# Kernel tuning notes

Hardware: AMD Instinct MI355X
Metric: run time of the kernel (lower is better)

Reference implementation:

```python
import jax, jax.numpy as jnp
import numpy as np

D_MODEL = 1024
N_HEADS = 16
HEAD_DIM = D_MODEL // N_HEADS
BATCH = 1
SEQLEN = 4096


def setup_inputs() -> dict:
    key = jax.random.key(0)
    k1, k2, k3 = jax.random.split(key, 3)
    x = jax.random.normal(k1, (BATCH, SEQLEN, D_MODEL), dtype=jnp.float32)
    # match typical Dense init scale so softmax isn't saturated
    Wqkv = jax.random.normal(k2, (D_MODEL, 3 * D_MODEL), dtype=jnp.float32) / np.sqrt(D_MODEL)
    Wout = jax.random.normal(k3, (D_MODEL, D_MODEL), dtype=jnp.float32) / np.sqrt(D_MODEL)
    return {"x": x, "Wqkv": Wqkv, "Wout": Wout}


def reference(x, Wqkv, Wout):
    b, l, d = x.shape
    qkv = x @ Wqkv  # [b, l, 3d]
    q, k, v = jnp.split(qkv, 3, axis=-1)
    # [b, l, d] -> [b, h, l, hd]
    def to_heads(t):
        return t.reshape(b, l, N_HEADS, HEAD_DIM).transpose(0, 2, 1, 3)
    q, k, v = to_heads(q), to_heads(k), to_heads(v)
    scale = 1.0 / np.sqrt(HEAD_DIM)
    attn = jnp.einsum('bhld,bhsd->bhls', q, k) * scale  # [b,h,l,l]
    causal_mask = jnp.tril(jnp.ones((l, l), dtype=bool))
    attn = jnp.where(causal_mask, attn, -jnp.inf)
    attn = jax.nn.softmax(attn, axis=-1)
    out = jnp.einsum('bhls,bhsd->bhld', attn, v)  # [b,h,l,hd]
    out = out.transpose(0, 2, 1, 3).reshape(b, l, d)
    return out @ Wout
```

## Files before the change

### kernel.cpp

```cpp
#include <hip/hip_runtime.h>

#define SEQ 4096
#define DM 1024
#define NH 16
#define HD 64

typedef __attribute__((ext_vector_type(8))) short short8;
typedef __attribute__((ext_vector_type(4))) short short4v;
typedef __attribute__((ext_vector_type(2))) short short2v;
typedef __attribute__((ext_vector_type(4))) float float4v;
typedef __attribute__((ext_vector_type(4))) int int4v;

__device__ __forceinline__ short f2bf(float f) {
    union { float f; unsigned u; } v; v.f = f;
    unsigned u = v.u;
    return (short)((u + 0x7fffu + ((u >> 16) & 1u)) >> 16);
}
__device__ __forceinline__ int cvtpk(float lo, float hi) {
    int r;
    asm("v_cvt_pk_bf16_f32 %0, %1, %2" : "=v"(r) : "v"(lo), "v"(hi));
    return r;
}

__device__ __forceinline__ void gload_lds16(const void* g, void* l) {
    __builtin_amdgcn_global_load_lds(
        (const __attribute__((address_space(1))) void*)g,
        (__attribute__((address_space(3))) void*)l, 16, 0, 0);
}

__global__ void cast_x(const float* __restrict__ in, short* __restrict__ out, int n4) {
    int i = blockIdx.x * blockDim.x + threadIdx.x;
    if (i < n4) {
        float4v x = ((const float4v*)in)[i];
        short4v o;
        o[0] = f2bf(x[0]); o[1] = f2bf(x[1]); o[2] = f2bf(x[2]); o[3] = f2bf(x[3]);
        ((short4v*)out)[i] = o;
    }
}

__global__ void transpose_cast(const float* __restrict__ in, short* __restrict__ out,
                               int H, int W, int scaled_rows, float scale) {
    __shared__ float tile[32][33];
    int bx = blockIdx.x * 32, by = blockIdx.y * 32;
    int tx = threadIdx.x, ty = threadIdx.y;
#pragma unroll
    for (int i = 0; i < 32; i += 8)
        tile[ty + i][tx] = in[(by + ty + i) * W + bx + tx];
    __syncthreads();
#pragma unroll
    for (int i = 0; i < 32; i += 8) {
        int orow = bx + ty + i;
        float sc = (orow < scaled_rows) ? scale : 1.0f;
        out[orow * H + by + tx] = f2bf(tile[tx][ty + i] * sc);
    }
}

__global__ void transpose_v(const short* __restrict__ qkv, short* __restrict__ vt) {
    __shared__ short tile[64][66];
    int h = blockIdx.z;
    int l0 = blockIdx.x * 64;
    int tx = threadIdx.x, ty = threadIdx.y;
#pragma unroll
    for (int i = 0; i < 8; i++) {
        int r = ty + i * 8;
        short2v v = *(const short2v*)&qkv[(l0 + r) * (3 * DM) + 2 * DM + h * HD + 2 * tx];
        tile[r][2 * tx] = v[0];
        tile[r][2 * tx + 1] = v[1];
    }
    __syncthreads();
#pragma unroll
    for (int i = 0; i < 8; i++) {
        int d = ty + i * 8;
        short2v v;
        v[0] = tile[2 * tx][d];
        v[1] = tile[2 * tx + 1][d];
        int s = l0 + 2 * tx;
        int soff = (s & ~31) | ((s & 12) << 1) | ((s & 16) >> 2) | (s & 3);
        *(short2v*)&vt[(h * HD + d) * SEQ + soff] = v;
    }
}

template <typename OutT>
__global__ __launch_bounds__(256) void gemm_bt(const short* __restrict__ A,
                                               const short* __restrict__ BT,
                                               OutT* __restrict__ C,
                                               int M, int N, int K) {
    __shared__ short As[128 * 32];
    __shared__ short Bs[128 * 32];
    int tid  = threadIdx.x;
    int m0   = blockIdx.y * 128;
    int n0   = blockIdx.x * 128;
    int w    = tid >> 6, lane = tid & 63;
    int wm   = w >> 1,  wn   = w & 1;
    int quad = lane >> 4, l15 = lane & 15;
    int srow = lane >> 2;
    int scol = (lane & 3) * 8;

    float4v acc[4][4];
#pragma unroll
    for (int mi = 0; mi < 4; mi++)
#pragma unroll
        for (int ni = 0; ni < 4; ni++)
            acc[mi][ni] = {0.f, 0.f, 0.f, 0.f};

    for (int k0 = 0; k0 < K; k0 += 32) {
        __syncthreads();
#pragma unroll
        for (int t = 0; t < 2; t++) {
            int chunk = w * 2 + t;
            int r = chunk * 16 + srow;
            gload_lds16(&A[(m0 + r) * K + k0 + scol], &As[chunk * 16 * 32]);
            gload_lds16(&BT[(n0 + r) * K + k0 + scol], &Bs[chunk * 16 * 32]);
        }
        __syncthreads();
        short8 a[4], b[4];
#pragma unroll
        for (int mi = 0; mi < 4; mi++)
            a[mi] = *(const short8*)&As[(wm * 64 + mi * 16 + l15) * 32 + quad * 8];
#pragma unroll
        for (int ni = 0; ni < 4; ni++)
            b[ni] = *(const short8*)&Bs[(wn * 64 + ni * 16 + l15) * 32 + quad * 8];
#pragma unroll
        for (int mi = 0; mi < 4; mi++)
#pragma unroll
            for (int ni = 0; ni < 4; ni++)
                acc[mi][ni] = __builtin_amdgcn_mfma_f32_16x16x32_bf16(a[mi], b[ni], acc[mi][ni], 0, 0, 0);
    }

#pragma unroll
    for (int mi = 0; mi < 4; mi++)
#pragma unroll
        for (int ni = 0; ni < 4; ni++)
#pragma unroll
            for (int r = 0; r < 4; r++) {
                int row = m0 + wm * 64 + mi * 16 + quad * 4 + r;
                int col = n0 + wn * 64 + ni * 16 + l15;
                float v = acc[mi][ni][r];
                if constexpr (sizeof(OutT) == 2) C[row * N + col] = (OutT)f2bf(v);
                else                             C[row * N + col] = (OutT)v;
            }
}

__global__ __launch_bounds__(256) void gemm_bt64(const short* __restrict__ A,
                                                 const short* __restrict__ BT,
                                                 float* __restrict__ C,
                                                 int M, int N, int K) {
    __shared__ short As[64 * 32];
    __shared__ short Bs[128 * 32];
    int tid  = threadIdx.x;
    int m0   = blockIdx.y * 64;
    int n0   = blockIdx.x * 128;
    int w    = tid >> 6, lane = tid & 63;
    int wm   = w >> 1,  wn   = w & 1;
    int quad = lane >> 4, l15 = lane & 15;
    int srow = lane >> 2;
    int scol = (lane & 3) * 8;

    float4v acc[2][4];
#pragma unroll
    for (int mi = 0; mi < 2; mi++)
#pragma unroll
        for (int ni = 0; ni < 4; ni++)
            acc[mi][ni] = {0.f, 0.f, 0.f, 0.f};

    for (int k0 = 0; k0 < K; k0 += 32) {
        __syncthreads();
        {
            int r = w * 16 + srow;
            gload_lds16(&A[(m0 + r) * K + k0 + scol], &As[w * 16 * 32]);
        }
#pragma unroll
        for (int t = 0; t < 2; t++) {
            int chunk = w * 2 + t;
            int r = chunk * 16 + srow;
            gload_lds16(&BT[(n0 + r) * K + k0 + scol], &Bs[chunk * 16 * 32]);
        }
        __syncthreads();
        short8 a[2], b[4];
#pragma unroll
        for (int mi = 0; mi < 2; mi++)
            a[mi] = *(const short8*)&As[(wm * 32 + mi * 16 + l15) * 32 + quad * 8];
#pragma unroll
        for (int ni = 0; ni < 4; ni++)
            b[ni] = *(const short8*)&Bs[(wn * 64 + ni * 16 + l15) * 32 + quad * 8];
#pragma unroll
        for (int mi = 0; mi < 2; mi++)
#pragma unroll
            for (int ni = 0; ni < 4; ni++)
                acc[mi][ni] = __builtin_amdgcn_mfma_f32_16x16x32_bf16(a[mi], b[ni], acc[mi][ni], 0, 0, 0);
    }

#pragma unroll
    for (int mi = 0; mi < 2; mi++)
#pragma unroll
        for (int ni = 0; ni < 4; ni++)
#pragma unroll
            for (int r = 0; r < 4; r++) {
                int row = m0 + wm * 32 + mi * 16 + quad * 4 + r;
                int col = n0 + wn * 64 + ni * 16 + l15;
                C[row * N + col] = acc[mi][ni][r];
            }
}

__global__ __launch_bounds__(256, 2) void attn_kernel(const short* __restrict__ qkv,
                                                      const short* __restrict__ vtp,
                                                      float* __restrict__ Of0,
                                                      float* __restrict__ Of1,
                                                      float* __restrict__ Of2,
                                                      float* __restrict__ Lf0,
                                                      float* __restrict__ Lf1,
                                                      float* __restrict__ Lf2) {
    __shared__ short Ks[3][64 * 64];
    __shared__ short Vs[3][64 * 64];
    int gid = blockIdx.x;
    int rr = gid & 7, qq = gid >> 3;
    int hb = qq / 48;
    int rem = qq - hb * 48;
    int h = rr + 8 * hb;
    int b = rem & 15;
    int j = rem >> 4;
    float* __restrict__ Of = (j == 0) ? Of0 : (j == 1) ? Of1 : Of2;
    float* __restrict__ Lf = (j == 0) ? Lf0 : (j == 1) ? Lf1 : Lf2;
    int B0 = 2 * b + 2;

    int tid = threadIdx.x;
    int w = tid >> 6, lane = tid & 63;
    int quad = lane >> 4, l15 = lane & 15;
    int rowb = w * 16;
    int lrow = lane >> 3;
    int cg   = (lane & 7) ^ lrow;
    int xr   = (l15 & 7) * 8;

    const short* Kg = qkv + DM + h * HD;
    const short* Vg = vtp + (h * HD) * SEQ;

    short8 onesv;
#pragma unroll
    for (int i = 0; i < 8; i++) onesv[i] = (short)0x3F80;

#pragma unroll 1
    for (int sg = 0; sg < 2; sg++) {
        int t, st0, stN;
        if (sg == 0) {
            t = b;
            st0 = 22 * j;
            stN = (22 * j + 22 < B0) ? 22 * j + 22 : B0;
        } else {
            t = 31 - b;
            int a0 = 22 * j - B0;
            st0 = (a0 > 0) ? a0 : 0;
            stN = 22 * j + 22 - B0;
        }
        if (st0 >= stN) continue;

        int q0 = t * 128;
        int qw = q0 + w * 32;

        short8 aq[2][2];
#pragma unroll
        for (int mi = 0; mi < 2; mi++)
#pragma unroll
            for (int kk = 0; kk < 2; kk++)
                aq[mi][kk] = *(const short8*)&qkv[(qw + mi * 16 + l15) * (3 * DM) + h * HD + kk * 32 + quad * 8];

        float4v lacc[2];
        float4v o[2][4];
#pragma unroll
        for (int mi = 0; mi < 2; mi++) {
            lacc[mi] = {0.f, 0.f, 0.f, 0.f};
#pragma unroll
            for (int dt = 0; dt < 4; dt++)
                o[mi][dt] = {0.f, 0.f, 0.f, 0.f};
        }

        auto stage = [&](int slot, int tt_) {
            int s0_ = tt_ * 64;
#pragma unroll
            for (int i = 0; i < 2; i++) {
                int r = rowb + i * 8;
                gload_lds16(&Kg[(s0_ + r + lrow) * (3 * DM) + cg * 8], &Ks[slot][r * 64]);
                gload_lds16(&Vg[(r + lrow) * SEQ + s0_ + cg * 8],      &Vs[slot][r * 64]);
            }
        };

        stage(0, st0);
        bool two = (st0 + 1 < stN);
        if (two) {
            stage(1, st0 + 1);
            asm volatile("s_waitcnt vmcnt(4)" ::: "memory");
        } else {
            asm volatile("s_waitcnt vmcnt(0)" ::: "memory");
        }
        __builtin_amdgcn_s_barrier();
        __builtin_amdgcn_sched_barrier(0);

        short8 pa_p[2][2];
        short8 vc_p[8];
        int si = 0;
        for (int tt = st0; tt < stN; tt++) {
            int s0 = tt * 64;
            int s2 = si + 2; if (s2 >= 3) s2 -= 3;
            bool haveStage = (tt + 2 < stN);
            if (haveStage) stage(s2, tt + 2);

            const short* Kb = &Ks[si][0];
            const short* Vb = &Vs[si][0];

            short8 kc[8];
#pragma unroll
            for (int ni = 0; ni < 4; ni++)
#pragma unroll
                for (int kk = 0; kk < 2; kk++)
                    kc[ni * 2 + kk] = *(const short8*)&Kb[(ni * 16 + l15) * 64 + (((kk * 4 + quad) * 8) ^ xr)];

            if (tt > st0) {
                __builtin_amdgcn_s_setprio(1);
#pragma unroll
                for (int mi = 0; mi < 2; mi++)
#pragma unroll
                    for (int pr = 0; pr < 2; pr++)
                        lacc[mi] = __builtin_amdgcn_mfma_f32_16x16x32_bf16(pa_p[mi][pr], onesv, lacc[mi], 0, 0, 0);
#pragma unroll
                for (int mi = 0; mi < 2; mi++)
#pragma unroll
                    for (int dt = 0; dt < 4; dt++)
#pragma unroll
                        for (int pr = 0; pr < 2; pr++)
                            o[mi][dt] = __builtin_amdgcn_mfma_f32_16x16x32_bf16(pa_p[mi][pr], vc_p[dt * 2 + pr], o[mi][dt], 0, 0, 0);
                __builtin_amdgcn_s_setprio(0);
            }

#pragma unroll
            for (int dt = 0; dt < 4; dt++)
#pragma unroll
                for (int pr = 0; pr < 2; pr++)
                    vc_p[dt * 2 + pr] = *(const short8*)&Vb[(dt * 16 + l15) * 64 + (((pr * 4 + quad) * 8) ^ xr)];

            float4v s[2][4];
            __builtin_amdgcn_s_setprio(1);
#pragma unroll
            for (int mi = 0; mi < 2; mi++)
#pragma unroll
                for (int ni = 0; ni < 4; ni++) {
                    float4v a = {0.f, 0.f, 0.f, 0.f};
#pragma unroll
                    for (int kk = 0; kk < 2; kk++)
                        a = __builtin_amdgcn_mfma_f32_16x16x32_bf16(kc[ni * 2 + kk], aq[mi][kk], a, 0, 0, 0);
                    s[mi][ni] = a;
                }
            __builtin_amdgcn_s_setprio(0);

            bool diag = (s0 + 63 > qw);
            if (diag) {
#pragma unroll
                for (int mi = 0; mi < 2; mi++) {
                    int qrow = qw + mi * 16 + l15;
#pragma unroll
                    for (int ni = 0; ni < 4; ni++)
#pragma unroll
                        for (int r = 0; r < 4; r++) {
                            float p = __builtin_amdgcn_exp2f(s[mi][ni][r]);
                            int scol = s0 + ni * 16 + quad * 4 + r;
                            s[mi][ni][r] = (scol <= qrow) ? p : 0.f;
                        }
                }
            } else {
#pragma unroll
                for (int mi = 0; mi < 2; mi++)
#pragma unroll
                    for (int ni = 0; ni < 4; ni++)
#pragma unroll
                        for (int r = 0; r < 4; r++)
                            s[mi][ni][r] = __builtin_amdgcn_exp2f(s[mi][ni][r]);
            }
#pragma unroll
            for (int mi = 0; mi < 2; mi++)
#pragma unroll
                for (int pr = 0; pr < 2; pr++) {
                    int4v wpk;
                    wpk[0] = cvtpk(s[mi][2 * pr][0], s[mi][2 * pr][1]);
                    wpk[1] = cvtpk(s[mi][2 * pr][2], s[mi][2 * pr][3]);
                    wpk[2] = cvtpk(s[mi][2 * pr + 1][0], s[mi][2 * pr + 1][1]);
                    wpk[3] = cvtpk(s[mi][2 * pr + 1][2], s[mi][2 * pr + 1][3]);
                    pa_p[mi][pr] = *(short8*)&wpk;
                }

            asm volatile("s_waitcnt lgkmcnt(0)" ::: "memory");
            if (haveStage) asm volatile("s_waitcnt vmcnt(4)" ::: "memory");
            else           asm volatile("s_waitcnt vmcnt(0)" ::: "memory");
            __builtin_amdgcn_s_barrier();
            __builtin_amdgcn_sched_barrier(0);
            si = si + 1; if (si >= 3) si = 0;
        }

        __builtin_amdgcn_s_setprio(1);
#pragma unroll
        for (int mi = 0; mi < 2; mi++)
#pragma unroll
            for (int pr = 0; pr < 2; pr++)
                lacc[mi] = __builtin_amdgcn_mfma_f32_16x16x32_bf16(pa_p[mi][pr], onesv, lacc[mi], 0, 0, 0);
#pragma unroll
        for (int mi = 0; mi < 2; mi++)
#pragma unroll
            for (int dt = 0; dt < 4; dt++)
#pragma unroll
                for (int pr = 0; pr < 2; pr++)
                    o[mi][dt] = __builtin_amdgcn_mfma_f32_16x16x32_bf16(pa_p[mi][pr], vc_p[dt * 2 + pr], o[mi][dt], 0, 0, 0);
        __builtin_amdgcn_s_setprio(0);

#pragma unroll
        for (int mi = 0; mi < 2; mi++)
#pragma unroll
            for (int r = 0; r < 4; r++) {
                int row = qw + mi * 16 + quad * 4 + r;
#pragma unroll
                for (int dt = 0; dt < 4; dt++)
                    Of[row * DM + h * HD + dt * 16 + l15] = o[mi][dt][r];
            }
        if (l15 == 0) {
#pragma unroll
            for (int mi = 0; mi < 2; mi++)
#pragma unroll
                for (int r = 0; r < 4; r++)
                    Lf[h * SEQ + qw + mi * 16 + quad * 4 + r] = lacc[mi][r];
        }
    }
}

__global__ void attn_finalize(const float* __restrict__ Of0, const float* __restrict__ Of1,
                              const float* __restrict__ Of2,
                              const float* __restrict__ Lf0, const float* __restrict__ Lf1,
                              const float* __restrict__ Lf2,
                              short* __restrict__ ao) {
    int i = blockIdx.x * blockDim.x + threadIdx.x;
    int q  = i >> 8;
    int c4 = i & 255;
    int h  = c4 >> 4;
    int t  = q >> 7;
    bool lowq = (t < 16);
    int b = lowq ? t : 31 - t;
    bool use0 = lowq || (b <= 9);
    bool use1 = (!lowq) || (b >= 11);
    bool use2 = !lowq;

    float l = 0.f;
    float4v acc = {0.f, 0.f, 0.f, 0.f};
    if (use0) {
        l += Lf0[h * SEQ + q];
        float4v a = ((const float4v*)Of0)[i];
        acc[0] += a[0]; acc[1] += a[1]; acc[2] += a[2]; acc[3] += a[3];
    }
    if (use1) {
        l += Lf1[h * SEQ + q];
        float4v a = ((const float4v*)Of1)[i];
        acc[0] += a[0]; acc[1] += a[1]; acc[2] += a[2]; acc[3] += a[3];
    }
    if (use2) {
        l += Lf2[h * SEQ + q];
        float4v a = ((const float4v*)Of2)[i];
        acc[0] += a[0]; acc[1] += a[1]; acc[2] += a[2]; acc[3] += a[3];
    }
    float inv = 1.0f / l;
    short4v o;
    o[0] = f2bf(acc[0] * inv);
    o[1] = f2bf(acc[1] * inv);
    o[2] = f2bf(acc[2] * inv);
    o[3] = f2bf(acc[3] * inv);
    ((short4v*)ao)[i] = o;
}

extern "C" void kernel_launch(void* const* d_in, const int* in_sizes, int n_in,
                              void* d_out, int out_size, void* d_ws, size_t ws_size,
                              hipStream_t stream) {
    const float* x    = (const float*)d_in[0];
    const float* Wqkv = (const float*)d_in[1];
    const float* Wout = (const float*)d_in[2];
    float* out = (float*)d_out;

    char* ws = (char*)d_ws;
    short* xb    = (short*)(ws);
    short* wqkvT = (short*)(ws + 8388608);
    float* Of0   = (float*)(ws);
    float* Of1   = (float*)(d_out);
    short* qkv   = (short*)(ws + 16777216);
    short* vt    = (short*)(ws + 41943040);
    short* ao    = (short*)(ws + 50331648);
    float* Of2   = (float*)(ws + 58720256);
    float* Lf0   = (float*)(ws + 75497472);
    float* Lf1   = (float*)(ws + 75759616);
    float* Lf2   = (float*)(ws + 76021760);
    short* woutT = (short*)(ws + 76283904);

    const float SC = 0.18033688011112042f;

    cast_x<<<4096, 256, 0, stream>>>(x, xb, (SEQ * DM) / 4);
    transpose_cast<<<dim3(3 * DM / 32, DM / 32), dim3(32, 8), 0, stream>>>(Wqkv, wqkvT, DM, 3 * DM, DM, SC);
    transpose_cast<<<dim3(DM / 32, DM / 32), dim3(32, 8), 0, stream>>>(Wout, woutT, DM, DM, 0, 1.0f);

    gemm_bt<short><<<dim3(3 * DM / 128, SEQ / 128), 256, 0, stream>>>(xb, wqkvT, qkv, SEQ, 3 * DM, DM);

    transpose_v<<<dim3(SEQ / 64, 1, NH), dim3(32, 8), 0, stream>>>(qkv, vt);

    attn_kernel<<<768, 256, 0, stream>>>(qkv, vt, Of0, Of1, Of2, Lf0, Lf1, Lf2);
    attn_finalize<<<(SEQ * DM / 4) / 256, 256, 0, stream>>>(Of0, Of1, Of2, Lf0, Lf1, Lf2, ao);

    gemm_bt64<<<dim3(DM / 128, SEQ / 64), 256, 0, stream>>>(ao, woutT, out, SEQ, DM, DM);
}
```

Measured before the change: 204.0 us.

## Split attention tile into halves interleaving QK, PV MFMAs and softmax; compute row sums on VALU

Splits each 64-key tile's QK^T, exp and PV work into two 32-column halves, with sched_barriers so the MFMAs of one half overlap the exp/pack work and V fragment loads of the other. The softmax denominator was computed with extra MFMAs against a ones vector. It now comes from per-lane VALU accumulation plus a cross-quad shuffle reduction at the end. This frees matrix-core cycles and shortens dependency chains, in exchange for more VALU adds and rigid scheduling that may limit compiler freedom.

```diff
diff --git a/kernel.cpp b/kernel.cpp
--- a/kernel.cpp
+++ b/kernel.cpp
@@ -234,10 +234,6 @@
     const short* Kg = qkv + DM + h * HD;
     const short* Vg = vtp + (h * HD) * SEQ;
 
-    short8 onesv;
-#pragma unroll
-    for (int i = 0; i < 8; i++) onesv[i] = (short)0x3F80;
-
 #pragma unroll 1
     for (int sg = 0; sg < 2; sg++) {
         int t, st0, stN;
@@ -263,15 +259,13 @@
             for (int kk = 0; kk < 2; kk++)
                 aq[mi][kk] = *(const short8*)&qkv[(qw + mi * 16 + l15) * (3 * DM) + h * HD + kk * 32 + quad * 8];
 
-        float4v lacc[2];
+        float lp[2] = {0.f, 0.f};
         float4v o[2][4];
 #pragma unroll
-        for (int mi = 0; mi < 2; mi++) {
-            lacc[mi] = {0.f, 0.f, 0.f, 0.f};
+        for (int mi = 0; mi < 2; mi++)
 #pragma unroll
             for (int dt = 0; dt < 4; dt++)
                 o[mi][dt] = {0.f, 0.f, 0.f, 0.f};
-        }
 
         auto stage = [&](int slot, int tt_) {
             int s0_ = tt_ * 64;
@@ -301,10 +295,12 @@
             int s0 = tt * 64;
             int s2 = si + 2; if (s2 >= 3) s2 -= 3;
             bool haveStage = (tt + 2 < stN);
+            bool havePrev  = (tt > st0);
             if (haveStage) stage(s2, tt + 2);
 
             const short* Kb = &Ks[si][0];
             const short* Vb = &Vs[si][0];
+            bool diag = (s0 + 63 > qw);
 
             short8 kc[8];
 #pragma unroll
@@ -313,35 +309,12 @@
                 for (int kk = 0; kk < 2; kk++)
                     kc[ni * 2 + kk] = *(const short8*)&Kb[(ni * 16 + l15) * 64 + (((kk * 4 + quad) * 8) ^ xr)];
 
-            if (tt > st0) {
-                __builtin_amdgcn_s_setprio(1);
-#pragma unroll
-                for (int mi = 0; mi < 2; mi++)
-#pragma unroll
-                    for (int pr = 0; pr < 2; pr++)
-                        lacc[mi] = __builtin_amdgcn_mfma_f32_16x16x32_bf16(pa_p[mi][pr], onesv, lacc[mi], 0, 0, 0);
-#pragma unroll
-                for (int mi = 0; mi < 2; mi++)
-#pragma unroll
-                    for (int dt = 0; dt < 4; dt++)
-#pragma unroll
-                        for (int pr = 0; pr < 2; pr++)
-                            o[mi][dt] = __builtin_amdgcn_mfma_f32_16x16x32_bf16(pa_p[mi][pr], vc_p[dt * 2 + pr], o[mi][dt], 0, 0, 0);
-                __builtin_amdgcn_s_setprio(0);
-            }
-
-#pragma unroll
-            for (int dt = 0; dt < 4; dt++)
-#pragma unroll
-                for (int pr = 0; pr < 2; pr++)
-                    vc_p[dt * 2 + pr] = *(const short8*)&Vb[(dt * 16 + l15) * 64 + (((pr * 4 + quad) * 8) ^ xr)];
-
             float4v s[2][4];
             __builtin_amdgcn_s_setprio(1);
 #pragma unroll
             for (int mi = 0; mi < 2; mi++)
 #pragma unroll
-                for (int ni = 0; ni < 4; ni++) {
+                for (int ni = 0; ni < 2; ni++) {
                     float4v a = {0.f, 0.f, 0.f, 0.f};
 #pragma unroll
                     for (int kk = 0; kk < 2; kk++)
@@ -349,41 +322,100 @@
                     s[mi][ni] = a;
                 }
             __builtin_amdgcn_s_setprio(0);
-
-            bool diag = (s0 + 63 > qw);
-            if (diag) {
-#pragma unroll
-                for (int mi = 0; mi < 2; mi++) {
-                    int qrow = qw + mi * 16 + l15;
-#pragma unroll
-                    for (int ni = 0; ni < 4; ni++)
-#pragma unroll
-                        for (int r = 0; r < 4; r++) {
-                            float p = __builtin_amdgcn_exp2f(s[mi][ni][r]);
+            __builtin_amdgcn_sched_barrier(0);
+
+            if (havePrev) {
+                __builtin_amdgcn_s_setprio(1);
+#pragma unroll
+                for (int mi = 0; mi < 2; mi++)
+#pragma unroll
+                    for (int dt = 0; dt < 4; dt++)
+                        o[mi][dt] = __builtin_amdgcn_mfma_f32_16x16x32_bf16(pa_p[mi][0], vc_p[dt * 2 + 0], o[mi][dt], 0, 0, 0);
+                __builtin_amdgcn_s_setprio(0);
+            }
+            __builtin_amdgcn_sched_barrier(0);
+
+#pragma unroll
+            for (int dt = 0; dt < 4; dt++)
+                vc_p[dt * 2 + 0] = *(const short8*)&Vb[(dt * 16 + l15) * 64 + (((0 * 4 + quad) * 8) ^ xr)];
+            __builtin_amdgcn_sched_barrier(0);
+
+#pragma unroll
+            for (int mi = 0; mi < 2; mi++) {
+                int qrow = qw + mi * 16 + l15;
+#pragma unroll
+                for (int ni = 0; ni < 2; ni++)
+#pragma unroll
+                    for (int r = 0; r < 4; r++) {
+                        float p = __builtin_amdgcn_exp2f(s[mi][ni][r]);
+                        if (diag) {
                             int scol = s0 + ni * 16 + quad * 4 + r;
-                            s[mi][ni][r] = (scol <= qrow) ? p : 0.f;
+                            p = (scol <= qrow) ? p : 0.f;
                         }
+                        lp[mi] += p;
+                        s[mi][ni][r] = p;
+                    }
+                int4v wpk;
+                wpk[0] = cvtpk(s[mi][0][0], s[mi][0][1]);
+                wpk[1] = cvtpk(s[mi][0][2], s[mi][0][3]);
+                wpk[2] = cvtpk(s[mi][1][0], s[mi][1][1]);
+                wpk[3] = cvtpk(s[mi][1][2], s[mi][1][3]);
+                pa_p[mi][0] = *(short8*)&wpk;
+            }
+            __builtin_amdgcn_sched_barrier(0);
+
+            __builtin_amdgcn_s_setprio(1);
+#pragma unroll
+            for (int mi = 0; mi < 2; mi++)
+#pragma unroll
+                for (int ni = 2; ni < 4; ni++) {
+                    float4v a = {0.f, 0.f, 0.f, 0.f};
+#pragma unroll
+                    for (int kk = 0; kk < 2; kk++)
+                        a = __builtin_amdgcn_mfma_f32_16x16x32_bf16(kc[ni * 2 + kk], aq[mi][kk], a, 0, 0, 0);
+                    s[mi][ni] = a;
                 }
-            } else {
+            __builtin_amdgcn_s_setprio(0);
+            __builtin_amdgcn_sched_barrier(0);
+
+            if (havePrev) {
+                __builtin_amdgcn_s_setprio(1);
 #pragma unroll
                 for (int mi = 0; mi < 2; mi++)
 #pragma unroll
-                    for (int ni = 0; ni < 4; ni++)
-#pragma unroll
-                        for (int r = 0; r < 4; r++)
-                            s[mi][ni][r] = __builtin_amdgcn_exp2f(s[mi][ni][r]);
-            }
-#pragma unroll
-            for (int mi = 0; mi < 2; mi++)
-#pragma unroll
-                for (int pr = 0; pr < 2; pr++) {
-                    int4v wpk;
-                    wpk[0] = cvtpk(s[mi][2 * pr][0], s[mi][2 * pr][1]);
-                    wpk[1] = cvtpk(s[mi][2 * pr][2], s[mi][2 * pr][3]);
-                    wpk[2] = cvtpk(s[mi][2 * pr + 1][0], s[mi][2 * pr + 1][1]);
-                    wpk[3] = cvtpk(s[mi][2 * pr + 1][2], s[mi][2 * pr + 1][3]);
-                    pa_p[mi][pr] = *(short8*)&wpk;
-                }
+                    for (int dt = 0; dt < 4; dt++)
+                        o[mi][dt] = __builtin_amdgcn_mfma_f32_16x16x32_bf16(pa_p[mi][1], vc_p[dt * 2 + 1], o[mi][dt], 0, 0, 0);
+                __builtin_amdgcn_s_setprio(0);
+            }
+            __builtin_amdgcn_sched_barrier(0);
+
+#pragma unroll
+            for (int dt = 0; dt < 4; dt++)
+                vc_p[dt * 2 + 1] = *(const short8*)&Vb[(dt * 16 + l15) * 64 + (((1 * 4 + quad) * 8) ^ xr)];
+            __builtin_amdgcn_sched_barrier(0);
+
+#pragma unroll
+            for (int mi = 0; mi < 2; mi++) {
+                int qrow = qw + mi * 16 + l15;
+#pragma unroll
+                for (int ni = 2; ni < 4; ni++)
+#pragma unroll
+                    for (int r = 0; r < 4; r++) {
+                        float p = __builtin_amdgcn_exp2f(s[mi][ni][r]);
+                        if (diag) {
+                            int scol = s0 + ni * 16 + quad * 4 + r;
+                            p = (scol <= qrow) ? p : 0.f;
+                        }
+                        lp[mi] += p;
+                        s[mi][ni][r] = p;
+                    }
+                int4v wpk;
+                wpk[0] = cvtpk(s[mi][2][0], s[mi][2][1]);
+                wpk[1] = cvtpk(s[mi][2][2], s[mi][2][3]);
+                wpk[2] = cvtpk(s[mi][3][0], s[mi][3][1]);
+                wpk[3] = cvtpk(s[mi][3][2], s[mi][3][3]);
+                pa_p[mi][1] = *(short8*)&wpk;
+            }
 
             asm volatile("s_waitcnt lgkmcnt(0)" ::: "memory");
             if (haveStage) asm volatile("s_waitcnt vmcnt(4)" ::: "memory");
@@ -397,11 +429,6 @@
 #pragma unroll
         for (int mi = 0; mi < 2; mi++)
 #pragma unroll
-            for (int pr = 0; pr < 2; pr++)
-                lacc[mi] = __builtin_amdgcn_mfma_f32_16x16x32_bf16(pa_p[mi][pr], onesv, lacc[mi], 0, 0, 0);
-#pragma unroll
-        for (int mi = 0; mi < 2; mi++)
-#pragma unroll
             for (int dt = 0; dt < 4; dt++)
 #pragma unroll
                 for (int pr = 0; pr < 2; pr++)
@@ -409,6 +436,11 @@
         __builtin_amdgcn_s_setprio(0);
 
 #pragma unroll
+        for (int mi = 0; mi < 2; mi++) {
+            lp[mi] += __shfl_xor(lp[mi], 16, 64);
+            lp[mi] += __shfl_xor(lp[mi], 32, 64);
+        }
+#pragma unroll
         for (int mi = 0; mi < 2; mi++)
 #pragma unroll
             for (int r = 0; r < 4; r++) {
@@ -417,12 +449,10 @@
                 for (int dt = 0; dt < 4; dt++)
                     Of[row * DM + h * HD + dt * 16 + l15] = o[mi][dt][r];
             }
-        if (l15 == 0) {
+        if (quad == 0) {
 #pragma unroll
             for (int mi = 0; mi < 2; mi++)
-#pragma unroll
-                for (int r = 0; r < 4; r++)
-                    Lf[h * SEQ + qw + mi * 16 + quad * 4 + r] = lacc[mi][r];
+                Lf[h * SEQ + qw + mi * 16 + l15] = lp[mi];
         }
     }
 }
```

After: 217.7 us. 6.7% more time.
